# Kernel optimization log

Hardware: AMD Instinct MI355X
Metric: run time of the kernel (lower is better)

Reference implementation:

```python
import jax, jax.numpy as jnp
import numpy as np
import math

B, S, N, D, H = 4, 64, 256, 512, 8
DEPTH = D // H

def setup_inputs() -> dict:
    key = jax.random.key(0)
    ks = jax.random.split(key, 9)
    scale = 1.0 / math.sqrt(D)
    return {
        "x": jax.random.normal(ks[0], (B, S, N, D), dtype=jnp.float32),
        "Wq": jax.random.normal(ks[1], (D, D), dtype=jnp.float32) * scale,
        "bq": jax.random.normal(ks[2], (D,), dtype=jnp.float32) * 0.01,
        "Wk": jax.random.normal(ks[3], (D, D), dtype=jnp.float32) * scale,
        "bk": jax.random.normal(ks[4], (D,), dtype=jnp.float32) * 0.01,
        "Wv": jax.random.normal(ks[5], (D, D), dtype=jnp.float32) * scale,
        "bv": jax.random.normal(ks[6], (D,), dtype=jnp.float32) * 0.01,
        "Wo": jax.random.normal(ks[7], (D, D), dtype=jnp.float32) * scale,
        "bo": jax.random.normal(ks[8], (D,), dtype=jnp.float32) * 0.01,
    }

def _split_heads(t):
    # (B, S, M, D) -> (B, H, S, M, depth); matches split_head.forward (4D path)
    # followed by the att_dim==2 permute(0, 2, 1, 3, 4) in cross_attention.
    b, s, m, _ = t.shape
    return t.reshape(b, s, m, H, DEPTH).transpose(0, 3, 1, 2, 4)

def reference(x, Wq, bq, Wk, bk, Wv, bv, Wo, bo):
    b, s, n, d = x.shape
    # att_dim == 2: query is the cls token along the joint/patch axis.
    q = _split_heads(x[:, :, 0:1, :] @ Wq + bq)   # (B, H, S, 1, depth)
    k = _split_heads(x @ Wk + bk)                  # (B, H, S, N, depth)
    v = _split_heads(x @ Wv + bv)                  # (B, H, S, N, depth)
    # scaled dot product attention (mask is None in cross_attention)
    logits = jnp.einsum('bhsqd,bhskd->bhsqk', q, k) / math.sqrt(DEPTH)
    attn = jax.nn.softmax(logits, axis=-1)         # (B, H, S, 1, N)
    ctx = jnp.einsum('bhsqk,bhskd->bhsqd', attn, v)  # (B, H, S, 1, depth)
    # permute(0, 2, 3, 1, 4) then reshape (B, S, 1, D)
    concat = ctx.transpose(0, 2, 3, 1, 4).reshape(b, s, 1, d)
    return concat @ Wo + bo
```

## Files before the change

### kernel.cpp

```cpp
#include <hip/hip_runtime.h>
#include <stdint.h>


__device__ __forceinline__ void gemm_ks_body(
    const float* __restrict__ A, long a_row_stride, int a_col_off_mult,
    const float* __restrict__ W, const float* __restrict__ bias,
    float* __restrict__ C, int rt, int jt, int t,
    float (*a_s)[512], float (*red_s)[4][64]) {
  const int w = t >> 6, lane = t & 63;

#pragma unroll
  for (int l = 0; l < 2; ++l) {
    int flat4 = t + l * 256;
    int arow = flat4 >> 7;
    int k4 = (flat4 & 127) * 4;
    float4 v = *(const float4*)&A[(long)(rt * 4 + arow) * a_row_stride +
                                  (long)jt * a_col_off_mult + k4];
    a_s[arow][k4] = v.x; a_s[arow][k4 + 1] = v.y;
    a_s[arow][k4 + 2] = v.z; a_s[arow][k4 + 3] = v.w;
  }
  __syncthreads();

  const int j = jt * 64 + lane;
  float acc0 = 0.f, acc1 = 0.f, acc2 = 0.f, acc3 = 0.f;
  const float* wp = W + (long)(w * 128) * 512 + j;
  const float* ap = &a_s[0][w * 128];
#pragma unroll 8
  for (int k = 0; k < 128; ++k) {
    float wv = wp[(long)k * 512];
    acc0 += ap[k] * wv;
    acc1 += ap[512 + k] * wv;
    acc2 += ap[1024 + k] * wv;
    acc3 += ap[1536 + k] * wv;
  }
  if (w > 0) {
    red_s[w - 1][0][lane] = acc0;
    red_s[w - 1][1][lane] = acc1;
    red_s[w - 1][2][lane] = acc2;
    red_s[w - 1][3][lane] = acc3;
  }
  __syncthreads();
  if (w == 0) {
#pragma unroll
    for (int rr = 0; rr < 3; ++rr) {
      acc0 += red_s[rr][0][lane];
      acc1 += red_s[rr][1][lane];
      acc2 += red_s[rr][2][lane];
      acc3 += red_s[rr][3][lane];
    }
    const float b = bias[j];
    C[(long)(rt * 4 + 0) * 512 + j] = acc0 + b;
    C[(long)(rt * 4 + 1) * 512 + j] = acc1 + b;
    C[(long)(rt * 4 + 2) * 512 + j] = acc2 + b;
    C[(long)(rt * 4 + 3) * 512 + j] = acc3 + b;
  }
}

__global__ __launch_bounds__(256) void prep_kernel(
    const float* __restrict__ x, const float* __restrict__ Wq,
    const float* __restrict__ bq, const float* __restrict__ Wk,
    float* __restrict__ WkT, float* __restrict__ q) {
  __shared__ float a_s[4][512];
  __shared__ float red_s[3][4][64];
  const int t = threadIdx.x;

  if (blockIdx.x < 256) {
    float (*tile)[64] = (float(*)[64])&a_s[0][0];
    const int j0 = (blockIdx.x & 15) * 32;
    const int c0 = (blockIdx.x >> 4) * 32;
    {
      const int row = t >> 3;
      const int c4 = (t & 7) * 4;
      float4 v = *(const float4*)&Wk[(long)(j0 + row) * 512 + c0 + c4];
      float* tr = &tile[0][0] + row * 33;
      tr[c4] = v.x; tr[c4 + 1] = v.y; tr[c4 + 2] = v.z; tr[c4 + 3] = v.w;
    }
    __syncthreads();
    {
      const int row = t >> 3;
      const int j4 = (t & 7) * 4;
      const float* tb = &tile[0][0];
      float4 v = make_float4(tb[j4 * 33 + row], tb[(j4 + 1) * 33 + row],
                             tb[(j4 + 2) * 33 + row], tb[(j4 + 3) * 33 + row]);
      *(float4*)&WkT[(long)(c0 + row) * 512 + j0 + j4] = v;
    }
  } else {
    const int bid = blockIdx.x - 256;
    const int rt = bid & 63;
    const int jt = bid >> 6;
    gemm_ks_body(x, 131072L, 0, Wq, bq, q, rt, jt, t, a_s, red_s);
  }
}

__global__ __launch_bounds__(256) void gemm_ks_kernel(
    const float* __restrict__ A, long a_row_stride, int a_col_off_mult,
    const float* __restrict__ W, const float* __restrict__ bias,
    float* __restrict__ C) {
  __shared__ float a_s[4][512];
  __shared__ float red_s[3][4][64];
  gemm_ks_body(A, a_row_stride, a_col_off_mult, W, bias, C,
               blockIdx.x, blockIdx.y, threadIdx.x, a_s, red_s);
}

__global__ __launch_bounds__(256) void r_kernel(
    const float* __restrict__ q, const float* __restrict__ WkT,
    float* __restrict__ r_all) {
  const int rt = blockIdx.x;
  const int h = blockIdx.y;
  const int t = threadIdx.x;
  __shared__ float q_s[4][64];

  {
    int row = t >> 6, c = t & 63;
    q_s[row][c] = q[(long)(rt * 4 + row) * 512 + h * 64 + c];
  }
  __syncthreads();

  const int jp4 = (t & 127) * 4;
  const int rh = t >> 7;
  float4 acc0 = make_float4(0.f, 0.f, 0.f, 0.f);
  float4 acc1 = make_float4(0.f, 0.f, 0.f, 0.f);
#pragma unroll 8
  for (int c = 0; c < 64; ++c) {
    float4 w4 = *(const float4*)&WkT[(long)(h * 64 + c) * 512 + jp4];
    float q0 = q_s[rh * 2][c], q1 = q_s[rh * 2 + 1][c];
    acc0.x += q0 * w4.x; acc0.y += q0 * w4.y; acc0.z += q0 * w4.z; acc0.w += q0 * w4.w;
    acc1.x += q1 * w4.x; acc1.y += q1 * w4.y; acc1.z += q1 * w4.z; acc1.w += q1 * w4.w;
  }
  *(float4*)&r_all[(long)(rt * 4 + rh * 2) * 4096 + h * 512 + jp4] = acc0;
  *(float4*)&r_all[(long)(rt * 4 + rh * 2 + 1) * 4096 + h * 512 + jp4] = acc1;
}

__global__ __launch_bounds__(1024) void attn_kernel(
    const float* __restrict__ x, const float* __restrict__ r_all,
    float* __restrict__ Y) {
  const int bs = blockIdx.x;
  const int t = threadIdx.x;
  const int w = t >> 6, lane = t & 63;
  __shared__ float p_s[8][256];
  __shared__ float yp[8][512];

  float rv[8][8];
  const float* rb = r_all + (long)bs * 4096 + lane * 8;
#pragma unroll
  for (int h = 0; h < 8; ++h) {
    float4 a = *(const float4*)&rb[h * 512];
    float4 b = *(const float4*)&rb[h * 512 + 4];
    rv[h][0] = a.x; rv[h][1] = a.y; rv[h][2] = a.z; rv[h][3] = a.w;
    rv[h][4] = b.x; rv[h][5] = b.y; rv[h][6] = b.z; rv[h][7] = b.w;
  }

  const int l4 = lane & 4, l2 = lane & 2, l1 = lane & 1;
#pragma unroll 4
  for (int i = 0; i < 16; ++i) {
    const int n = w * 16 + i;
    const float* xr = x + ((long)bs * 256 + n) * 512 + lane * 8;
    float4 xa = *(const float4*)xr;
    float4 xb = *(const float4*)(xr + 4);
    float acc[8];
#pragma unroll
    for (int h = 0; h < 8; ++h)
      acc[h] = xa.x * rv[h][0] + xa.y * rv[h][1] + xa.z * rv[h][2] + xa.w * rv[h][3]
             + xb.x * rv[h][4] + xb.y * rv[h][5] + xb.z * rv[h][6] + xb.w * rv[h][7];
#pragma unroll
    for (int j = 0; j < 4; ++j) {
      float v = l4 ? acc[j] : acc[j + 4];
      float tt = __shfl_xor(v, 4);
      acc[j] = (l4 ? acc[j + 4] : acc[j]) + tt;
    }
#pragma unroll
    for (int j = 0; j < 2; ++j) {
      float v = l2 ? acc[j] : acc[j + 2];
      float tt = __shfl_xor(v, 2);
      acc[j] = (l2 ? acc[j + 2] : acc[j]) + tt;
    }
    {
      float v = l1 ? acc[0] : acc[1];
      float tt = __shfl_xor(v, 1);
      acc[0] = (l1 ? acc[1] : acc[0]) + tt;
    }
    acc[0] += __shfl_xor(acc[0], 8);
    acc[0] += __shfl_xor(acc[0], 16);
    acc[0] += __shfl_xor(acc[0], 32);
    if (lane < 8)
      p_s[lane][n] = acc[0] * 0.125f;
  }
  __syncthreads();

  if (w < 8) {
    float4 lv = *(const float4*)&p_s[w][lane * 4];
    float m = fmaxf(fmaxf(lv.x, lv.y), fmaxf(lv.z, lv.w));
    for (int o = 32; o; o >>= 1) m = fmaxf(m, __shfl_xor(m, o));
    float e0 = __expf(lv.x - m), e1 = __expf(lv.y - m);
    float e2 = __expf(lv.z - m), e3 = __expf(lv.w - m);
    float s = e0 + e1 + e2 + e3;
    for (int o = 32; o; o >>= 1) s += __shfl_xor(s, o);
    const float inv = 1.f / s;
    *(float4*)&p_s[w][lane * 4] = make_float4(e0 * inv, e1 * inv, e2 * inv, e3 * inv);
  }
  __syncthreads();

  const int d = t & 511;
  const int half = t >> 9;
  float acc[8] = {};
  const float* xb2 = x + ((long)bs * 256 + half * 128) * 512 + d;
#pragma unroll 8
  for (int n = 0; n < 128; ++n) {
    float xv = xb2[(long)n * 512];
#pragma unroll
    for (int h = 0; h < 8; ++h)
      acc[h] += p_s[h][half * 128 + n] * xv;
  }
  if (half == 1) {
#pragma unroll
    for (int h = 0; h < 8; ++h) yp[h][d] = acc[h];
  }
  __syncthreads();
  if (half == 0) {
#pragma unroll
    for (int h = 0; h < 8; ++h)
      Y[(long)bs * 4096 + h * 512 + d] = acc[h] + yp[h][d];
  }
}

extern "C" void kernel_launch(void* const* d_in, const int* in_sizes, int n_in,
                              void* d_out, int out_size, void* d_ws, size_t ws_size,
                              hipStream_t stream) {
  (void)in_sizes; (void)n_in; (void)out_size; (void)ws_size;
  const float* x  = (const float*)d_in[0];
  const float* Wq = (const float*)d_in[1];
  const float* bq = (const float*)d_in[2];
  const float* Wk = (const float*)d_in[3];
  const float* bk = (const float*)d_in[4];  (void)bk;
  const float* Wv = (const float*)d_in[5];
  const float* bv = (const float*)d_in[6];
  const float* Wo = (const float*)d_in[7];
  const float* bo = (const float*)d_in[8];
  float* out = (float*)d_out;

  float* WkT = (float*)d_ws;
  float* q   = WkT + 262144;
  float* r   = q + 131072;
  float* Y   = r + 1048576;
  float* ctx = Y + 1048576;

  prep_kernel<<<768, 256, 0, stream>>>(x, Wq, bq, Wk, WkT, q);
  r_kernel<<<dim3(64, 8), 256, 0, stream>>>(q, WkT, r);
  attn_kernel<<<256, 1024, 0, stream>>>(x, r, Y);
  gemm_ks_kernel<<<dim3(64, 8), 256, 0, stream>>>(Y, 4096L, 512, Wv, bv, ctx);
  gemm_ks_kernel<<<dim3(64, 8), 256, 0, stream>>>(ctx, 512L, 0, Wo, bo, out);
}
```

Measured before the change: 262.7 us.

## Fuse whole cross-attention pipeline into one per-(b,s) kernel with online softmax

Replaces the five kernel launches with a single kernel, one block per (b,s). Each block computes q, the Wk-folded query vector, the attention logits, an online softmax over 32-row x tiles staged in shared memory, and the Wv/Wo projections, with no workspace round trips. Each x row is read from global memory once instead of twice and launch overhead drops. In exchange every block redundantly reads the full Wq, Wk, Wv and Wo (4 MB total per block, through cache), uses large shared memory that limits occupancy, and runs only 256 blocks.

```diff
diff --git a/kernel.cpp b/kernel.cpp
--- a/kernel.cpp
+++ b/kernel.cpp
@@ -1,252 +1,248 @@
 #include <hip/hip_runtime.h>
 #include <stdint.h>
-
-
-__device__ __forceinline__ void gemm_ks_body(
-    const float* __restrict__ A, long a_row_stride, int a_col_off_mult,
-    const float* __restrict__ W, const float* __restrict__ bias,
-    float* __restrict__ C, int rt, int jt, int t,
-    float (*a_s)[512], float (*red_s)[4][64]) {
-  const int w = t >> 6, lane = t & 63;
-
-#pragma unroll
-  for (int l = 0; l < 2; ++l) {
-    int flat4 = t + l * 256;
-    int arow = flat4 >> 7;
-    int k4 = (flat4 & 127) * 4;
-    float4 v = *(const float4*)&A[(long)(rt * 4 + arow) * a_row_stride +
-                                  (long)jt * a_col_off_mult + k4];
-    a_s[arow][k4] = v.x; a_s[arow][k4 + 1] = v.y;
-    a_s[arow][k4 + 2] = v.z; a_s[arow][k4 + 3] = v.w;
-  }
-  __syncthreads();
-
-  const int j = jt * 64 + lane;
-  float acc0 = 0.f, acc1 = 0.f, acc2 = 0.f, acc3 = 0.f;
-  const float* wp = W + (long)(w * 128) * 512 + j;
-  const float* ap = &a_s[0][w * 128];
-#pragma unroll 8
-  for (int k = 0; k < 128; ++k) {
-    float wv = wp[(long)k * 512];
-    acc0 += ap[k] * wv;
-    acc1 += ap[512 + k] * wv;
-    acc2 += ap[1024 + k] * wv;
-    acc3 += ap[1536 + k] * wv;
-  }
-  if (w > 0) {
-    red_s[w - 1][0][lane] = acc0;
-    red_s[w - 1][1][lane] = acc1;
-    red_s[w - 1][2][lane] = acc2;
-    red_s[w - 1][3][lane] = acc3;
-  }
-  __syncthreads();
-  if (w == 0) {
-#pragma unroll
-    for (int rr = 0; rr < 3; ++rr) {
-      acc0 += red_s[rr][0][lane];
-      acc1 += red_s[rr][1][lane];
-      acc2 += red_s[rr][2][lane];
-      acc3 += red_s[rr][3][lane];
-    }
-    const float b = bias[j];
-    C[(long)(rt * 4 + 0) * 512 + j] = acc0 + b;
-    C[(long)(rt * 4 + 1) * 512 + j] = acc1 + b;
-    C[(long)(rt * 4 + 2) * 512 + j] = acc2 + b;
-    C[(long)(rt * 4 + 3) * 512 + j] = acc3 + b;
-  }
-}
-
-__global__ __launch_bounds__(256) void prep_kernel(
-    const float* __restrict__ x, const float* __restrict__ Wq,
-    const float* __restrict__ bq, const float* __restrict__ Wk,
-    float* __restrict__ WkT, float* __restrict__ q) {
-  __shared__ float a_s[4][512];
-  __shared__ float red_s[3][4][64];
-  const int t = threadIdx.x;
-
-  if (blockIdx.x < 256) {
-    float (*tile)[64] = (float(*)[64])&a_s[0][0];
-    const int j0 = (blockIdx.x & 15) * 32;
-    const int c0 = (blockIdx.x >> 4) * 32;
-    {
-      const int row = t >> 3;
-      const int c4 = (t & 7) * 4;
-      float4 v = *(const float4*)&Wk[(long)(j0 + row) * 512 + c0 + c4];
-      float* tr = &tile[0][0] + row * 33;
-      tr[c4] = v.x; tr[c4 + 1] = v.y; tr[c4 + 2] = v.z; tr[c4 + 3] = v.w;
-    }
-    __syncthreads();
-    {
-      const int row = t >> 3;
-      const int j4 = (t & 7) * 4;
-      const float* tb = &tile[0][0];
-      float4 v = make_float4(tb[j4 * 33 + row], tb[(j4 + 1) * 33 + row],
-                             tb[(j4 + 2) * 33 + row], tb[(j4 + 3) * 33 + row]);
-      *(float4*)&WkT[(long)(c0 + row) * 512 + j0 + j4] = v;
-    }
-  } else {
-    const int bid = blockIdx.x - 256;
-    const int rt = bid & 63;
-    const int jt = bid >> 6;
-    gemm_ks_body(x, 131072L, 0, Wq, bq, q, rt, jt, t, a_s, red_s);
-  }
-}
-
-__global__ __launch_bounds__(256) void gemm_ks_kernel(
-    const float* __restrict__ A, long a_row_stride, int a_col_off_mult,
-    const float* __restrict__ W, const float* __restrict__ bias,
-    float* __restrict__ C) {
-  __shared__ float a_s[4][512];
-  __shared__ float red_s[3][4][64];
-  gemm_ks_body(A, a_row_stride, a_col_off_mult, W, bias, C,
-               blockIdx.x, blockIdx.y, threadIdx.x, a_s, red_s);
-}
-
-__global__ __launch_bounds__(256) void r_kernel(
-    const float* __restrict__ q, const float* __restrict__ WkT,
-    float* __restrict__ r_all) {
-  const int rt = blockIdx.x;
-  const int h = blockIdx.y;
-  const int t = threadIdx.x;
-  __shared__ float q_s[4][64];
-
-  {
-    int row = t >> 6, c = t & 63;
-    q_s[row][c] = q[(long)(rt * 4 + row) * 512 + h * 64 + c];
-  }
-  __syncthreads();
-
-  const int jp4 = (t & 127) * 4;
-  const int rh = t >> 7;
-  float4 acc0 = make_float4(0.f, 0.f, 0.f, 0.f);
-  float4 acc1 = make_float4(0.f, 0.f, 0.f, 0.f);
-#pragma unroll 8
-  for (int c = 0; c < 64; ++c) {
-    float4 w4 = *(const float4*)&WkT[(long)(h * 64 + c) * 512 + jp4];
-    float q0 = q_s[rh * 2][c], q1 = q_s[rh * 2 + 1][c];
-    acc0.x += q0 * w4.x; acc0.y += q0 * w4.y; acc0.z += q0 * w4.z; acc0.w += q0 * w4.w;
-    acc1.x += q1 * w4.x; acc1.y += q1 * w4.y; acc1.z += q1 * w4.z; acc1.w += q1 * w4.w;
-  }
-  *(float4*)&r_all[(long)(rt * 4 + rh * 2) * 4096 + h * 512 + jp4] = acc0;
-  *(float4*)&r_all[(long)(rt * 4 + rh * 2 + 1) * 4096 + h * 512 + jp4] = acc1;
-}
-
-__global__ __launch_bounds__(1024) void attn_kernel(
-    const float* __restrict__ x, const float* __restrict__ r_all,
-    float* __restrict__ Y) {
+#include <math.h>
+
+
+#define NT 32
+
+__global__ __launch_bounds__(512) void fused_kernel(
+    const float* __restrict__ x,
+    const float* __restrict__ Wq, const float* __restrict__ bq,
+    const float* __restrict__ Wk,
+    const float* __restrict__ Wv, const float* __restrict__ bv,
+    const float* __restrict__ Wo, const float* __restrict__ bo,
+    float* __restrict__ out) {
   const int bs = blockIdx.x;
   const int t = threadIdx.x;
   const int w = t >> 6, lane = t & 63;
-  __shared__ float p_s[8][256];
-  __shared__ float yp[8][512];
+  const float* xb = x + (long)bs * 131072;
+
+  __shared__ float x_tile[NT * 512];
+  __shared__ float r_s[4096];
+  __shared__ float y_s[8 * 520];
+  __shared__ float q_s[512];
+  __shared__ float x0_s[512];
+  __shared__ float ctx_s[512];
+  __shared__ float red_s[3][512];
+  __shared__ float pt_s[8][NT];
+  __shared__ float f_s[8], s_s[8];
+
+  if (t < 128) *(float4*)&x0_s[t * 4] = *(const float4*)&xb[t * 4];
+  __syncthreads();
+
+  {
+    const int j4 = (t & 127) * 4;
+    const int kq = t >> 7;
+    float4 a = make_float4(0.f, 0.f, 0.f, 0.f);
+    const float* wp = Wq + (long)(kq * 128) * 512 + j4;
+    const float* ap = &x0_s[kq * 128];
+#pragma unroll 8
+    for (int k = 0; k < 128; ++k) {
+      float4 wv = *(const float4*)&wp[(long)k * 512];
+      float av = ap[k];
+      a.x += av * wv.x; a.y += av * wv.y; a.z += av * wv.z; a.w += av * wv.w;
+    }
+    if (kq > 0) *(float4*)&red_s[kq - 1][j4] = a;
+    __syncthreads();
+    if (kq == 0) {
+#pragma unroll
+      for (int rr = 0; rr < 3; ++rr) {
+        float4 b = *(const float4*)&red_s[rr][j4];
+        a.x += b.x; a.y += b.y; a.z += b.z; a.w += b.w;
+      }
+      float4 bb = *(const float4*)&bq[j4];
+      a.x += bb.x; a.y += bb.y; a.z += bb.z; a.w += bb.w;
+      *(float4*)&q_s[j4] = a;
+    }
+  }
+  __syncthreads();
+
+  {
+    const float* wrow = Wk + (long)t * 512;
+    for (int h = 0; h < 8; ++h) {
+      float racc = 0.f;
+      const float* qp = &q_s[h * 64];
+#pragma unroll
+      for (int c4 = 0; c4 < 16; ++c4) {
+        float4 wv = *(const float4*)&wrow[h * 64 + c4 * 4];
+        racc += qp[c4 * 4 + 0] * wv.x + qp[c4 * 4 + 1] * wv.y +
+                qp[c4 * 4 + 2] * wv.z + qp[c4 * 4 + 3] * wv.w;
+      }
+      r_s[h * 512 + t] = racc;
+    }
+  }
+  __syncthreads();
 
   float rv[8][8];
-  const float* rb = r_all + (long)bs * 4096 + lane * 8;
 #pragma unroll
   for (int h = 0; h < 8; ++h) {
-    float4 a = *(const float4*)&rb[h * 512];
-    float4 b = *(const float4*)&rb[h * 512 + 4];
+    float4 a = *(const float4*)&r_s[h * 512 + lane * 8];
+    float4 b = *(const float4*)&r_s[h * 512 + lane * 8 + 4];
     rv[h][0] = a.x; rv[h][1] = a.y; rv[h][2] = a.z; rv[h][3] = a.w;
     rv[h][4] = b.x; rv[h][5] = b.y; rv[h][6] = b.z; rv[h][7] = b.w;
   }
 
+  float accy[8] = {0.f, 0.f, 0.f, 0.f, 0.f, 0.f, 0.f, 0.f};
+  float m_h = -INFINITY, s_h = 0.f;
   const int l4 = lane & 4, l2 = lane & 2, l1 = lane & 1;
+
+  for (int tile = 0; tile < 8; ++tile) {
+    {
+      const float* src = xb + (long)tile * NT * 512;
+#pragma unroll
+      for (int i = 0; i < 8; ++i) {
+        int f4 = t + i * 512;
+        *(float4*)&x_tile[f4 * 4] = *(const float4*)&src[f4 * 4];
+      }
+    }
+    __syncthreads();
+
+#pragma unroll
+    for (int i = 0; i < 4; ++i) {
+      const int nl = w * 4 + i;
+      const float* xr = &x_tile[nl * 512 + lane * 8];
+      float4 xa = *(const float4*)xr;
+      float4 xb4 = *(const float4*)(xr + 4);
+      float acc[8];
+#pragma unroll
+      for (int h = 0; h < 8; ++h)
+        acc[h] = xa.x * rv[h][0] + xa.y * rv[h][1] + xa.z * rv[h][2] + xa.w * rv[h][3]
+               + xb4.x * rv[h][4] + xb4.y * rv[h][5] + xb4.z * rv[h][6] + xb4.w * rv[h][7];
+#pragma unroll
+      for (int j = 0; j < 4; ++j) {
+        float v = l4 ? acc[j] : acc[j + 4];
+        float tt = __shfl_xor(v, 4);
+        acc[j] = (l4 ? acc[j + 4] : acc[j]) + tt;
+      }
+#pragma unroll
+      for (int j = 0; j < 2; ++j) {
+        float v = l2 ? acc[j] : acc[j + 2];
+        float tt = __shfl_xor(v, 2);
+        acc[j] = (l2 ? acc[j + 2] : acc[j]) + tt;
+      }
+      {
+        float v = l1 ? acc[0] : acc[1];
+        float tt = __shfl_xor(v, 1);
+        acc[0] = (l1 ? acc[1] : acc[0]) + tt;
+      }
+      acc[0] += __shfl_xor(acc[0], 8);
+      acc[0] += __shfl_xor(acc[0], 16);
+      acc[0] += __shfl_xor(acc[0], 32);
+      if (lane < 8) pt_s[lane][nl] = acc[0] * 0.125f;
+    }
+    __syncthreads();
+
+    {
+      float l = (lane < 32) ? pt_s[w][lane] : -INFINITY;
+      float tm = l;
+#pragma unroll
+      for (int o = 16; o; o >>= 1) tm = fmaxf(tm, __shfl_xor(tm, o));
+      float m_new = fmaxf(m_h, tm);
+      float e = __expf(l - m_new);
+      float ts = e;
+#pragma unroll
+      for (int o = 16; o; o >>= 1) ts += __shfl_xor(ts, o);
+      float f = __expf(m_h - m_new);
+      s_h = s_h * f + ts;
+      m_h = m_new;
+      if (lane == 0) f_s[w] = f;
+      if (lane < 32) pt_s[w][lane] = e;
+    }
+    __syncthreads();
+
+    {
+#pragma unroll
+      for (int h = 0; h < 8; ++h) accy[h] *= f_s[h];
 #pragma unroll 4
-  for (int i = 0; i < 16; ++i) {
-    const int n = w * 16 + i;
-    const float* xr = x + ((long)bs * 256 + n) * 512 + lane * 8;
-    float4 xa = *(const float4*)xr;
-    float4 xb = *(const float4*)(xr + 4);
-    float acc[8];
-#pragma unroll
-    for (int h = 0; h < 8; ++h)
-      acc[h] = xa.x * rv[h][0] + xa.y * rv[h][1] + xa.z * rv[h][2] + xa.w * rv[h][3]
-             + xb.x * rv[h][4] + xb.y * rv[h][5] + xb.z * rv[h][6] + xb.w * rv[h][7];
-#pragma unroll
-    for (int j = 0; j < 4; ++j) {
-      float v = l4 ? acc[j] : acc[j + 4];
-      float tt = __shfl_xor(v, 4);
-      acc[j] = (l4 ? acc[j + 4] : acc[j]) + tt;
-    }
-#pragma unroll
-    for (int j = 0; j < 2; ++j) {
-      float v = l2 ? acc[j] : acc[j + 2];
-      float tt = __shfl_xor(v, 2);
-      acc[j] = (l2 ? acc[j + 2] : acc[j]) + tt;
-    }
-    {
-      float v = l1 ? acc[0] : acc[1];
-      float tt = __shfl_xor(v, 1);
-      acc[0] = (l1 ? acc[1] : acc[0]) + tt;
-    }
-    acc[0] += __shfl_xor(acc[0], 8);
-    acc[0] += __shfl_xor(acc[0], 16);
-    acc[0] += __shfl_xor(acc[0], 32);
-    if (lane < 8)
-      p_s[lane][n] = acc[0] * 0.125f;
-  }
-  __syncthreads();
-
-  if (w < 8) {
-    float4 lv = *(const float4*)&p_s[w][lane * 4];
-    float m = fmaxf(fmaxf(lv.x, lv.y), fmaxf(lv.z, lv.w));
-    for (int o = 32; o; o >>= 1) m = fmaxf(m, __shfl_xor(m, o));
-    float e0 = __expf(lv.x - m), e1 = __expf(lv.y - m);
-    float e2 = __expf(lv.z - m), e3 = __expf(lv.w - m);
-    float s = e0 + e1 + e2 + e3;
-    for (int o = 32; o; o >>= 1) s += __shfl_xor(s, o);
-    const float inv = 1.f / s;
-    *(float4*)&p_s[w][lane * 4] = make_float4(e0 * inv, e1 * inv, e2 * inv, e3 * inv);
-  }
-  __syncthreads();
-
-  const int d = t & 511;
-  const int half = t >> 9;
-  float acc[8] = {};
-  const float* xb2 = x + ((long)bs * 256 + half * 128) * 512 + d;
+      for (int n4 = 0; n4 < 8; ++n4) {
+        float xv0 = x_tile[(n4 * 4 + 0) * 512 + t];
+        float xv1 = x_tile[(n4 * 4 + 1) * 512 + t];
+        float xv2 = x_tile[(n4 * 4 + 2) * 512 + t];
+        float xv3 = x_tile[(n4 * 4 + 3) * 512 + t];
+#pragma unroll
+        for (int h = 0; h < 8; ++h) {
+          float4 p4 = *(const float4*)&pt_s[h][n4 * 4];
+          accy[h] += p4.x * xv0 + p4.y * xv1 + p4.z * xv2 + p4.w * xv3;
+        }
+      }
+    }
+    __syncthreads();
+  }
+
+  if (lane == 0) s_s[w] = s_h;
+  __syncthreads();
+#pragma unroll
+  for (int h = 0; h < 8; ++h) y_s[h * 520 + t] = accy[h] * (1.f / s_s[h]);
+  __syncthreads();
+
+  {
+    const int o4 = (t & 127) * 4;
+    const int kq = t >> 7;
+    const int h0 = o4 >> 6;
+    float4 a = make_float4(0.f, 0.f, 0.f, 0.f);
+    const float* wp = Wv + (long)(kq * 128) * 512 + o4;
+    const float* yp = &y_s[h0 * 520 + kq * 128];
 #pragma unroll 8
-  for (int n = 0; n < 128; ++n) {
-    float xv = xb2[(long)n * 512];
-#pragma unroll
-    for (int h = 0; h < 8; ++h)
-      acc[h] += p_s[h][half * 128 + n] * xv;
-  }
-  if (half == 1) {
-#pragma unroll
-    for (int h = 0; h < 8; ++h) yp[h][d] = acc[h];
-  }
-  __syncthreads();
-  if (half == 0) {
-#pragma unroll
-    for (int h = 0; h < 8; ++h)
-      Y[(long)bs * 4096 + h * 512 + d] = acc[h] + yp[h][d];
+    for (int k = 0; k < 128; ++k) {
+      float4 wv = *(const float4*)&wp[(long)k * 512];
+      float yv = yp[k];
+      a.x += yv * wv.x; a.y += yv * wv.y; a.z += yv * wv.z; a.w += yv * wv.w;
+    }
+    if (kq > 0) *(float4*)&red_s[kq - 1][o4] = a;
+    __syncthreads();
+    if (kq == 0) {
+#pragma unroll
+      for (int rr = 0; rr < 3; ++rr) {
+        float4 b = *(const float4*)&red_s[rr][o4];
+        a.x += b.x; a.y += b.y; a.z += b.z; a.w += b.w;
+      }
+      float4 bb = *(const float4*)&bv[o4];
+      a.x += bb.x; a.y += bb.y; a.z += bb.z; a.w += bb.w;
+      *(float4*)&ctx_s[o4] = a;
+    }
+  }
+  __syncthreads();
+
+  {
+    const int j4 = (t & 127) * 4;
+    const int kq = t >> 7;
+    float4 a = make_float4(0.f, 0.f, 0.f, 0.f);
+    const float* wp = Wo + (long)(kq * 128) * 512 + j4;
+    const float* cp = &ctx_s[kq * 128];
+#pragma unroll 8
+    for (int k = 0; k < 128; ++k) {
+      float4 wv = *(const float4*)&wp[(long)k * 512];
+      float cv = cp[k];
+      a.x += cv * wv.x; a.y += cv * wv.y; a.z += cv * wv.z; a.w += cv * wv.w;
+    }
+    if (kq > 0) *(float4*)&red_s[kq - 1][j4] = a;
+    __syncthreads();
+    if (kq == 0) {
+#pragma unroll
+      for (int rr = 0; rr < 3; ++rr) {
+        float4 b = *(const float4*)&red_s[rr][j4];
+        a.x += b.x; a.y += b.y; a.z += b.z; a.w += b.w;
+      }
+      float4 bb = *(const float4*)&bo[j4];
+      a.x += bb.x; a.y += bb.y; a.z += bb.z; a.w += bb.w;
+      *(float4*)&out[(long)bs * 512 + j4] = a;
+    }
   }
 }
 
 extern "C" void kernel_launch(void* const* d_in, const int* in_sizes, int n_in,
                               void* d_out, int out_size, void* d_ws, size_t ws_size,
                               hipStream_t stream) {
-  (void)in_sizes; (void)n_in; (void)out_size; (void)ws_size;
+  (void)in_sizes; (void)n_in; (void)out_size; (void)d_ws; (void)ws_size;
   const float* x  = (const float*)d_in[0];
   const float* Wq = (const float*)d_in[1];
   const float* bq = (const float*)d_in[2];
   const float* Wk = (const float*)d_in[3];
-  const float* bk = (const float*)d_in[4];  (void)bk;
   const float* Wv = (const float*)d_in[5];
   const float* bv = (const float*)d_in[6];
   const float* Wo = (const float*)d_in[7];
   const float* bo = (const float*)d_in[8];
   float* out = (float*)d_out;
 
-  float* WkT = (float*)d_ws;
-  float* q   = WkT + 262144;
-  float* r   = q + 131072;
-  float* Y   = r + 1048576;
-  float* ctx = Y + 1048576;
-
-  prep_kernel<<<768, 256, 0, stream>>>(x, Wq, bq, Wk, WkT, q);
-  r_kernel<<<dim3(64, 8), 256, 0, stream>>>(q, WkT, r);
-  attn_kernel<<<256, 1024, 0, stream>>>(x, r, Y);
-  gemm_ks_kernel<<<dim3(64, 8), 256, 0, stream>>>(Y, 4096L, 512, Wv, bv, ctx);
-  gemm_ks_kernel<<<dim3(64, 8), 256, 0, stream>>>(ctx, 512L, 0, Wo, bo, out);
+  fused_kernel<<<256, 512, 0, stream>>>(x, Wq, bq, Wk, Wv, bv, Wo, bo, out);
 }
```

After: 288.7 us. +9.9%, slower.
